# Kernel optimization log

Measured on AMD Instinct MI355X. Metric: run time of the kernel, lower is better.

## Reference

```python
import jax, jax.numpy as jnp
import numpy as np

N_NODES = 50000
N_EDGES = 800000
IN_DIM = 128
OUT_DIM = 64
NEG_SLOPE = 0.01  # torch F.leaky_relu default


def setup_inputs() -> dict:
    key = jax.random.key(0)
    k1, k2, k3, k4, k5 = jax.random.split(key, 5)
    features = jax.random.normal(k1, (N_NODES, IN_DIM), dtype=jnp.float32)
    # xavier-ish scale for weights
    fc_w = jax.random.normal(k2, (OUT_DIM, IN_DIM), dtype=jnp.float32) * (1.0 / np.sqrt(IN_DIM))
    attn_w = jax.random.normal(k3, (2 * OUT_DIM,), dtype=jnp.float32) * (1.0 / np.sqrt(2 * OUT_DIM))
    src = jax.random.randint(k4, (N_EDGES,), 0, N_NODES, dtype=jnp.int32)
    dst = jax.random.randint(k5, (N_EDGES,), 0, N_NODES, dtype=jnp.int32)
    return {"features": features, "fc_w": fc_w, "attn_w": attn_w, "src": src, "dst": dst}


def reference(features, fc_w, attn_w, src, dst):
    n = features.shape[0]
    out_dim = fc_w.shape[0]
    # z = fc(features), [N, out_dim]
    z = features @ fc_w.T
    # attn_fc([z_src || z_dst]) = z_src @ w_src + z_dst @ w_dst
    a_src = z @ attn_w[:out_dim]   # [N]
    a_dst = z @ attn_w[out_dim:]   # [N]
    e = a_src[src] + a_dst[dst]    # [E] per-edge raw score
    e = jnp.where(e > 0, e, NEG_SLOPE * e)  # leaky_relu
    # edge softmax over incoming edges of each dst node
    e_max = jax.ops.segment_max(e, dst, num_segments=n)      # [N]
    w = jnp.exp(e - e_max[dst])                               # [E]
    denom = jax.ops.segment_sum(w, dst, num_segments=n)       # [N]
    # weighted neighbor sum: sum_e alpha_e * z[src_e]
    num = jax.ops.segment_sum(w[:, None] * z[src], dst, num_segments=n)  # [N, out_dim]
    h = num / jnp.where(denom > 0, denom, 1.0)[:, None]
    # activation = elu
    h = jax.nn.elu(h)
    return h
```

## Files before the change

kernel.cpp:

```cpp
#include <hip/hip_runtime.h>
#include <hip/hip_bf16.h>
#include <hip/hip_fp16.h>

#define N_NODES 50000
#define N_EDGES 800000
#define IN_DIM 128
#define OUT_DIM 64
#define NEG_SLOPE 0.01f
#define NEG_INF (-3.0e38f)

#define N_STRIPS (N_NODES / 16)
#define Z_BLOCKS ((N_STRIPS + 3) / 4)
#define E_I4 (N_EDGES / 4)

#define NB ((N_NODES + 127) / 128)
#define CAP_B 3072
#define CNT_STRIDE 16
#define EB 100
#define CHUNK_I4 (E_I4 / EB)

typedef __bf16 bf16x8 __attribute__((ext_vector_type(8)));
typedef float f32x4 __attribute__((ext_vector_type(4)));

__device__ __forceinline__ unsigned short f2bf_us(float f) {
  __hip_bfloat16 h = __float2bfloat16(f);
  return *reinterpret_cast<unsigned short*>(&h);
}
__device__ __forceinline__ bf16x8 pack_bf16(float4 lo, float4 hi) {
  union { bf16x8 v; unsigned short u[8]; } r;
  r.u[0] = f2bf_us(lo.x); r.u[1] = f2bf_us(lo.y);
  r.u[2] = f2bf_us(lo.z); r.u[3] = f2bf_us(lo.w);
  r.u[4] = f2bf_us(hi.x); r.u[5] = f2bf_us(hi.y);
  r.u[6] = f2bf_us(hi.z); r.u[7] = f2bf_us(hi.w);
  return r.v;
}
__device__ __forceinline__ float bflo(unsigned u) {
  return __uint_as_float(u << 16);
}
__device__ __forceinline__ float bfhi(unsigned u) {
  return __uint_as_float(u & 0xffff0000u);
}

__global__ __launch_bounds__(256) void gat_z_bucket(
    const float* __restrict__ feat, const float* __restrict__ fcw,
    const float* __restrict__ attnw, __hip_bfloat16* __restrict__ z,
    float* __restrict__ asrc, float* __restrict__ adst,
    const int* __restrict__ src, const int* __restrict__ dst,
    int* __restrict__ cnt, unsigned* __restrict__ pairs) {
  if (blockIdx.x >= Z_BLOCKS) {
    __shared__ int hist[NB];
    __shared__ int curs[NB];
    const int tid = threadIdx.x;
    const int i0 = (blockIdx.x - Z_BLOCKS) * CHUNK_I4;
    for (int i = tid; i < NB; i += 256) hist[i] = 0;
    __syncthreads();
    for (int t = i0 + tid; t < i0 + CHUNK_I4; t += 256) {
      int4 d = ((const int4*)dst)[t];
      atomicAdd(&hist[d.x >> 7], 1);
      atomicAdd(&hist[d.y >> 7], 1);
      atomicAdd(&hist[d.z >> 7], 1);
      atomicAdd(&hist[d.w >> 7], 1);
    }
    __syncthreads();
    for (int i = tid; i < NB; i += 256) {
      int h = hist[i];
      curs[i] = h ? atomicAdd(cnt + i * CNT_STRIDE, h) : 0;
    }
    __syncthreads();
    for (int t = i0 + tid; t < i0 + CHUNK_I4; t += 256) {
      int4 s = ((const int4*)src)[t];
      int4 d = ((const int4*)dst)[t];
#define BKT_PUT(dd, ss)                                                    \
  {                                                                        \
    int b = (dd) >> 7;                                                     \
    int r = atomicAdd(&curs[b], 1);                                        \
    if (r < CAP_B)                                                         \
      pairs[(size_t)b * CAP_B + r] =                                       \
          ((unsigned)((dd) & 127) << 16) | (unsigned)(ss);                 \
  }
      BKT_PUT(d.x, s.x)
      BKT_PUT(d.y, s.y)
      BKT_PUT(d.z, s.z)
      BKT_PUT(d.w, s.w)
#undef BKT_PUT
    }
    return;
  }

  const int lane = threadIdx.x & 63;
  const int m = lane & 15;
  const int quad = lane >> 4;
  const int wv = blockIdx.x * 4 + (threadIdx.x >> 6);
  if (wv >= N_STRIPS) return;
  const int n0 = wv * 16;

  bf16x8 bfrag[4][4];
#pragma unroll
  for (int t = 0; t < 4; ++t) {
    const float* wr = fcw + (size_t)(m + 16 * t) * IN_DIM + quad * 8;
#pragma unroll
    for (int c = 0; c < 4; ++c) {
      float4 lo = *(const float4*)(wr + c * 32);
      float4 hi = *(const float4*)(wr + c * 32 + 4);
      bfrag[t][c] = pack_bf16(lo, hi);
    }
  }

  f32x4 acc[4] = {{0.f, 0.f, 0.f, 0.f}, {0.f, 0.f, 0.f, 0.f},
                  {0.f, 0.f, 0.f, 0.f}, {0.f, 0.f, 0.f, 0.f}};
  const float* ar = feat + (size_t)(n0 + m) * IN_DIM + quad * 8;
#pragma unroll
  for (int c = 0; c < 4; ++c) {
    float4 lo = *(const float4*)(ar + c * 32);
    float4 hi = *(const float4*)(ar + c * 32 + 4);
    const bf16x8 af = pack_bf16(lo, hi);
#pragma unroll
    for (int t = 0; t < 4; ++t)
      acc[t] = __builtin_amdgcn_mfma_f32_16x16x32_bf16(af, bfrag[t][c],
                                                       acc[t], 0, 0, 0);
  }

#pragma unroll
  for (int t = 0; t < 4; ++t)
#pragma unroll
    for (int r = 0; r < 4; ++r)
      z[(size_t)(n0 + quad * 4 + r) * OUT_DIM + m + 16 * t] =
          __float2bfloat16(acc[t][r]);

  float aws[4], awd[4];
#pragma unroll
  for (int t = 0; t < 4; ++t) {
    aws[t] = attnw[m + 16 * t];
    awd[t] = attnw[OUT_DIM + m + 16 * t];
  }
  float ps[4], pd[4];
#pragma unroll
  for (int r = 0; r < 4; ++r) {
    float s = 0.f, d = 0.f;
#pragma unroll
    for (int t = 0; t < 4; ++t) {
      s = fmaf(acc[t][r], aws[t], s);
      d = fmaf(acc[t][r], awd[t], d);
    }
    ps[r] = s;
    pd[r] = d;
  }
#pragma unroll
  for (int off = 1; off < 16; off <<= 1) {
#pragma unroll
    for (int r = 0; r < 4; ++r) {
      ps[r] += __shfl_xor(ps[r], off, 64);
      pd[r] += __shfl_xor(pd[r], off, 64);
    }
  }
  if (m == 0) {
#pragma unroll
    for (int r = 0; r < 4; ++r) {
      asrc[n0 + quad * 4 + r] = ps[r];
      adst[n0 + quad * 4 + r] = pd[r];
    }
  }
}

__global__ __launch_bounds__(256) void gat_build_csr(
    const unsigned* __restrict__ pairs, const int* __restrict__ cnt,
    int* __restrict__ offsets, int* __restrict__ ssorted) {
  __shared__ int hist[128], exo[128], cur[128], wsum[4];
  const int b = blockIdx.x;
  const int tid = threadIdx.x;

  int ls = 0;
  for (int i = tid; i < b; i += 256) ls += cnt[i * CNT_STRIDE];
#pragma unroll
  for (int off = 32; off; off >>= 1) ls += __shfl_xor(ls, off, 64);
  if ((tid & 63) == 0) wsum[tid >> 6] = ls;
  if (tid < 128) hist[tid] = 0;
  __syncthreads();
  const int base = wsum[0] + wsum[1] + wsum[2] + wsum[3];

  const int c = min(cnt[b * CNT_STRIDE], CAP_B);
  const unsigned* bp = pairs + (size_t)b * CAP_B;
  for (int i = tid; i < c; i += 256) atomicAdd(&hist[bp[i] >> 16], 1);
  __syncthreads();

  if (tid < 128) exo[tid] = hist[tid];
  __syncthreads();
  for (int off = 1; off < 128; off <<= 1) {
    int u = (tid >= off && tid < 128) ? exo[tid - off] : 0;
    __syncthreads();
    if (tid < 128) exo[tid] += u;
    __syncthreads();
  }
  if (tid < 128) {
    const int ex = exo[tid] - hist[tid];
    cur[tid] = ex;
    const int node = b * 128 + tid;
    if (node < N_NODES) offsets[node] = base + ex;
  }
  if (b == NB - 1 && tid == 0) offsets[N_NODES] = base + c;
  __syncthreads();

  for (int i = tid; i < c; i += 256) {
    const unsigned p = bp[i];
    const int r = atomicAdd(&cur[p >> 16], 1);
    ssorted[base + r] = (int)(p & 0xFFFFu);
  }
}

__global__ __launch_bounds__(256) void gat_agg(
    const __hip_bfloat16* __restrict__ zb, const float* __restrict__ asrc,
    const float* __restrict__ adst, const int* __restrict__ offsets,
    const int* __restrict__ ssorted, float* __restrict__ out) {
  const int lane = threadIdx.x & 63;
  const int j = lane & 7;
  const int eg = lane >> 3;
  const int node = (blockIdx.x * blockDim.x + threadIdx.x) >> 6;
  if (node >= N_NODES) return;
  const uint4* __restrict__ zp4 = (const uint4*)zb;
  const int o0 = offsets[node];
  const int o1 = offsets[node + 1];
  float4* __restrict__ orow = (float4*)(out + (size_t)node * OUT_DIM);
  if (o0 == o1) {
    if (eg == 0) {
      const float4 zv = {0.f, 0.f, 0.f, 0.f};
      orow[2 * j] = zv;
      orow[2 * j + 1] = zv;
    }
    return;
  }
  const float ad = adst[node];

  float m = NEG_INF, dsum = 0.f;
  float acca[8] = {0.f, 0.f, 0.f, 0.f, 0.f, 0.f, 0.f, 0.f};
  float accb[8] = {0.f, 0.f, 0.f, 0.f, 0.f, 0.f, 0.f, 0.f};

  for (int base = o0; base < o1; base += 64) {
    const int cnt = min(64, o1 - base);
    int s = 0;
    float ev = NEG_INF;
    if (lane < cnt) {
      s = ssorted[base + lane];
      float v = asrc[s] + ad;
      ev = v > 0.f ? v : NEG_SLOPE * v;
    }
    float cm = ev;
#pragma unroll
    for (int off = 32; off; off >>= 1) cm = fmaxf(cm, __shfl_xor(cm, off, 64));
    const float nm = fmaxf(m, cm);
    const float scale = __expf(m - nm);
    dsum *= scale;
#pragma unroll
    for (int c = 0; c < 8; ++c) {
      acca[c] *= scale;
      accb[c] *= scale;
    }
    m = nm;

    const float w = (lane < cnt) ? __expf(ev - m) : 0.f;
    dsum += w;
    const unsigned pk =
        (unsigned)s |
        ((unsigned)__half_as_ushort(__float2half(w)) << 16);

    const int ngr = (cnt + 7) >> 3;
    for (int g = 0; g < ngr; g += 2) {
      const unsigned pa = __shfl(pk, 8 * g + eg, 64);
      const int sa = (int)(pa & 0xFFFFu);
      const float wa = __half2float(__ushort_as_half((unsigned short)(pa >> 16)));
      const uint4 ua = zp4[(size_t)sa * 8 + j];
      if (g + 1 < ngr) {
        const unsigned pb = __shfl(pk, 8 * (g + 1) + eg, 64);
        const int sb = (int)(pb & 0xFFFFu);
        const float wb =
            __half2float(__ushort_as_half((unsigned short)(pb >> 16)));
        const uint4 ub = zp4[(size_t)sb * 8 + j];
        accb[0] = fmaf(wb, bflo(ub.x), accb[0]);
        accb[1] = fmaf(wb, bfhi(ub.x), accb[1]);
        accb[2] = fmaf(wb, bflo(ub.y), accb[2]);
        accb[3] = fmaf(wb, bfhi(ub.y), accb[3]);
        accb[4] = fmaf(wb, bflo(ub.z), accb[4]);
        accb[5] = fmaf(wb, bfhi(ub.z), accb[5]);
        accb[6] = fmaf(wb, bflo(ub.w), accb[6]);
        accb[7] = fmaf(wb, bfhi(ub.w), accb[7]);
      }
      acca[0] = fmaf(wa, bflo(ua.x), acca[0]);
      acca[1] = fmaf(wa, bfhi(ua.x), acca[1]);
      acca[2] = fmaf(wa, bflo(ua.y), acca[2]);
      acca[3] = fmaf(wa, bfhi(ua.y), acca[3]);
      acca[4] = fmaf(wa, bflo(ua.z), acca[4]);
      acca[5] = fmaf(wa, bfhi(ua.z), acca[5]);
      acca[6] = fmaf(wa, bflo(ua.w), acca[6]);
      acca[7] = fmaf(wa, bfhi(ua.w), acca[7]);
    }
  }

  float acc[8];
#pragma unroll
  for (int c = 0; c < 8; ++c) acc[c] = acca[c] + accb[c];
#pragma unroll
  for (int off = 8; off < 64; off <<= 1)
#pragma unroll
    for (int c = 0; c < 8; ++c) acc[c] += __shfl_xor(acc[c], off, 64);
#pragma unroll
  for (int off = 32; off; off >>= 1) dsum += __shfl_xor(dsum, off, 64);

  if (eg == 0) {
    const float inv = 1.f / (dsum > 0.f ? dsum : 1.f);
    float4 r0, r1;
    float h;
    h = acc[0] * inv; r0.x = h > 0.f ? h : expm1f(h);
    h = acc[1] * inv; r0.y = h > 0.f ? h : expm1f(h);
    h = acc[2] * inv; r0.z = h > 0.f ? h : expm1f(h);
    h = acc[3] * inv; r0.w = h > 0.f ? h : expm1f(h);
    h = acc[4] * inv; r1.x = h > 0.f ? h : expm1f(h);
    h = acc[5] * inv; r1.y = h > 0.f ? h : expm1f(h);
    h = acc[6] * inv; r1.z = h > 0.f ? h : expm1f(h);
    h = acc[7] * inv; r1.w = h > 0.f ? h : expm1f(h);
    orow[2 * j] = r0;
    orow[2 * j + 1] = r1;
  }
}

extern "C" void kernel_launch(void* const* d_in, const int* in_sizes, int n_in,
                              void* d_out, int out_size, void* d_ws, size_t ws_size,
                              hipStream_t stream) {
  const float* feat  = (const float*)d_in[0];
  const float* fcw   = (const float*)d_in[1];
  const float* attnw = (const float*)d_in[2];
  const int* src     = (const int*)d_in[3];
  const int* dst     = (const int*)d_in[4];
  float* out = (float*)d_out;

  char* ws = (char*)d_ws;
  __hip_bfloat16* z = (__hip_bfloat16*)ws;
  ws += (size_t)N_NODES * OUT_DIM * sizeof(__hip_bfloat16);
  float* asrc = (float*)ws;   ws += (size_t)N_NODES * sizeof(float);
  float* adst = (float*)ws;   ws += (size_t)N_NODES * sizeof(float);
  int* cnt = (int*)ws;        ws += (size_t)NB * CNT_STRIDE * sizeof(int);
  int* offsets = (int*)ws;    ws += (size_t)(N_NODES + 4) * sizeof(int);
  unsigned* pairs = (unsigned*)ws; ws += (size_t)NB * CAP_B * sizeof(unsigned);
  int* ssorted = (int*)ws;    ws += (size_t)N_EDGES * sizeof(int);

  hipMemsetAsync(cnt, 0, (size_t)NB * CNT_STRIDE * sizeof(int), stream);

  gat_z_bucket<<<Z_BLOCKS + EB, 256, 0, stream>>>(
      feat, fcw, attnw, z, asrc, adst, src, dst, cnt, pairs);
  gat_build_csr<<<NB, 256, 0, stream>>>(pairs, cnt, offsets, ssorted);
  gat_agg<<<(N_NODES * 64 + 255) / 256, 256, 0, stream>>>(z, asrc, adst,
                                                          offsets, ssorted, out);
}
```

Measured before the change: 145.8 us.

## Fuse CSR build and aggregation into one kernel with LDS-local sorted edges

Merges the CSR-building kernel and the aggregation kernel into a single kernel in which each block takes a 64-node bucket, counting-sorts its edges into LDS, gathers asrc values into LDS, and runs a three-pass (max, exp-sum, weighted sum) softmax aggregation per node. This removes one launch and the global round trip of offsets and the sorted source array, and drops the online-rescaling and fp16 weight packing. In exchange, buckets shrink to 64 nodes with a capacity of 1600 edges, and each block's waves handle 16 nodes serially, which lowers parallelism and loses the two-way gather unroll.

Result: slower. 166.1 us (+13.9%).

```diff
diff --git a/kernel.cpp b/kernel.cpp
--- a/kernel.cpp
+++ b/kernel.cpp
@@ -1,6 +1,5 @@
 #include <hip/hip_runtime.h>
 #include <hip/hip_bf16.h>
-#include <hip/hip_fp16.h>
 
 #define N_NODES 50000
 #define N_EDGES 800000
@@ -13,8 +12,9 @@
 #define Z_BLOCKS ((N_STRIPS + 3) / 4)
 #define E_I4 (N_EDGES / 4)
 
-#define NB ((N_NODES + 127) / 128)
-#define CAP_B 3072
+#define B_NODES 64
+#define NB ((N_NODES + B_NODES - 1) / B_NODES)
+#define CAP_B 1600
 #define CNT_STRIDE 16
 #define EB 100
 #define CHUNK_I4 (E_I4 / EB)
@@ -56,10 +56,10 @@
     __syncthreads();
     for (int t = i0 + tid; t < i0 + CHUNK_I4; t += 256) {
       int4 d = ((const int4*)dst)[t];
-      atomicAdd(&hist[d.x >> 7], 1);
-      atomicAdd(&hist[d.y >> 7], 1);
-      atomicAdd(&hist[d.z >> 7], 1);
-      atomicAdd(&hist[d.w >> 7], 1);
+      atomicAdd(&hist[d.x >> 6], 1);
+      atomicAdd(&hist[d.y >> 6], 1);
+      atomicAdd(&hist[d.z >> 6], 1);
+      atomicAdd(&hist[d.w >> 6], 1);
     }
     __syncthreads();
     for (int i = tid; i < NB; i += 256) {
@@ -72,11 +72,11 @@
       int4 d = ((const int4*)dst)[t];
 #define BKT_PUT(dd, ss)                                                    \
   {                                                                        \
-    int b = (dd) >> 7;                                                     \
+    int b = (dd) >> 6;                                                     \
     int r = atomicAdd(&curs[b], 1);                                        \
     if (r < CAP_B)                                                         \
       pairs[(size_t)b * CAP_B + r] =                                       \
-          ((unsigned)((dd) & 127) << 16) | (unsigned)(ss);                 \
+          ((unsigned)((dd) & 63) << 16) | (unsigned)(ss);                  \
   }
       BKT_PUT(d.x, s.x)
       BKT_PUT(d.y, s.y)
@@ -162,162 +162,142 @@
   }
 }
 
-__global__ __launch_bounds__(256) void gat_build_csr(
+__global__ __launch_bounds__(256) void gat_build_agg(
     const unsigned* __restrict__ pairs, const int* __restrict__ cnt,
-    int* __restrict__ offsets, int* __restrict__ ssorted) {
-  __shared__ int hist[128], exo[128], cur[128], wsum[4];
+    const float* __restrict__ asrc, const float* __restrict__ adst,
+    const __hip_bfloat16* __restrict__ zb, float* __restrict__ out) {
+  __shared__ int hist[B_NODES], exo[B_NODES], cur[B_NODES];
+  __shared__ unsigned short lsorted[CAP_B];
+  __shared__ float avs[CAP_B];
+  __shared__ float adl[B_NODES];
   const int b = blockIdx.x;
   const int tid = threadIdx.x;
-
-  int ls = 0;
-  for (int i = tid; i < b; i += 256) ls += cnt[i * CNT_STRIDE];
-#pragma unroll
-  for (int off = 32; off; off >>= 1) ls += __shfl_xor(ls, off, 64);
-  if ((tid & 63) == 0) wsum[tid >> 6] = ls;
-  if (tid < 128) hist[tid] = 0;
-  __syncthreads();
-  const int base = wsum[0] + wsum[1] + wsum[2] + wsum[3];
+  const int lane = tid & 63;
+  const int wv = tid >> 6;
+
+  if (tid < B_NODES) {
+    hist[tid] = 0;
+    const int node = b * B_NODES + tid;
+    adl[tid] = (node < N_NODES) ? adst[node] : 0.f;
+  }
+  __syncthreads();
 
   const int c = min(cnt[b * CNT_STRIDE], CAP_B);
   const unsigned* bp = pairs + (size_t)b * CAP_B;
   for (int i = tid; i < c; i += 256) atomicAdd(&hist[bp[i] >> 16], 1);
   __syncthreads();
 
-  if (tid < 128) exo[tid] = hist[tid];
-  __syncthreads();
-  for (int off = 1; off < 128; off <<= 1) {
-    int u = (tid >= off && tid < 128) ? exo[tid - off] : 0;
-    __syncthreads();
-    if (tid < 128) exo[tid] += u;
-    __syncthreads();
-  }
-  if (tid < 128) {
-    const int ex = exo[tid] - hist[tid];
-    cur[tid] = ex;
-    const int node = b * 128 + tid;
-    if (node < N_NODES) offsets[node] = base + ex;
-  }
-  if (b == NB - 1 && tid == 0) offsets[N_NODES] = base + c;
+  if (wv == 0) {
+    const int v = hist[lane];
+    int incl = v;
+#pragma unroll
+    for (int off = 1; off < 64; off <<= 1) {
+      int u = __shfl_up(incl, off, 64);
+      if (lane >= off) incl += u;
+    }
+    exo[lane] = incl - v;
+    cur[lane] = incl - v;
+  }
   __syncthreads();
 
   for (int i = tid; i < c; i += 256) {
     const unsigned p = bp[i];
     const int r = atomicAdd(&cur[p >> 16], 1);
-    ssorted[base + r] = (int)(p & 0xFFFFu);
-  }
-}
-
-__global__ __launch_bounds__(256) void gat_agg(
-    const __hip_bfloat16* __restrict__ zb, const float* __restrict__ asrc,
-    const float* __restrict__ adst, const int* __restrict__ offsets,
-    const int* __restrict__ ssorted, float* __restrict__ out) {
-  const int lane = threadIdx.x & 63;
+    lsorted[r] = (unsigned short)(p & 0xFFFFu);
+  }
+  __syncthreads();
+
+  for (int i = tid; i < c; i += 256) avs[i] = asrc[lsorted[i]];
+  __syncthreads();
+
+  const uint4* __restrict__ zp4 = (const uint4*)zb;
   const int j = lane & 7;
   const int eg = lane >> 3;
-  const int node = (blockIdx.x * blockDim.x + threadIdx.x) >> 6;
-  if (node >= N_NODES) return;
-  const uint4* __restrict__ zp4 = (const uint4*)zb;
-  const int o0 = offsets[node];
-  const int o1 = offsets[node + 1];
-  float4* __restrict__ orow = (float4*)(out + (size_t)node * OUT_DIM);
-  if (o0 == o1) {
+
+#pragma unroll 1
+  for (int it = 0; it < 16; ++it) {
+    const int ln = 4 * it + wv;
+    const int node = b * B_NODES + ln;
+    if (node >= N_NODES) continue;
+    const int base = exo[ln];
+    const int cn = hist[ln];
+    float4* __restrict__ orow = (float4*)(out + (size_t)node * OUT_DIM);
+    if (cn == 0) {
+      if (eg == 0) {
+        const float4 zv = {0.f, 0.f, 0.f, 0.f};
+        orow[2 * j] = zv;
+        orow[2 * j + 1] = zv;
+      }
+      continue;
+    }
+    const float ad = adl[ln];
+
+    float m = NEG_INF;
+    for (int e0 = 0; e0 < cn; e0 += 64) {
+      const int e = e0 + lane;
+      float ev = NEG_INF;
+      if (e < cn) {
+        const float v = avs[base + e] + ad;
+        ev = v > 0.f ? v : NEG_SLOPE * v;
+        avs[base + e] = ev;
+      }
+#pragma unroll
+      for (int off = 32; off; off >>= 1)
+        ev = fmaxf(ev, __shfl_xor(ev, off, 64));
+      m = fmaxf(m, ev);
+    }
+    float dsum = 0.f;
+    for (int e0 = 0; e0 < cn; e0 += 64) {
+      const int e = e0 + lane;
+      float w = 0.f;
+      if (e < cn) {
+        w = __expf(avs[base + e] - m);
+        avs[base + e] = w;
+      }
+      dsum += w;
+    }
+#pragma unroll
+    for (int off = 32; off; off >>= 1) dsum += __shfl_xor(dsum, off, 64);
+
+    float acc[8] = {0.f, 0.f, 0.f, 0.f, 0.f, 0.f, 0.f, 0.f};
+    for (int e0 = 0; e0 < cn; e0 += 8) {
+      const int e = e0 + eg;
+      float w = 0.f;
+      int s = 0;
+      if (e < cn) {
+        w = avs[base + e];
+        s = lsorted[base + e];
+      }
+      const uint4 u = zp4[(size_t)s * 8 + j];
+      acc[0] = fmaf(w, bflo(u.x), acc[0]);
+      acc[1] = fmaf(w, bfhi(u.x), acc[1]);
+      acc[2] = fmaf(w, bflo(u.y), acc[2]);
+      acc[3] = fmaf(w, bfhi(u.y), acc[3]);
+      acc[4] = fmaf(w, bflo(u.z), acc[4]);
+      acc[5] = fmaf(w, bfhi(u.z), acc[5]);
+      acc[6] = fmaf(w, bflo(u.w), acc[6]);
+      acc[7] = fmaf(w, bfhi(u.w), acc[7]);
+    }
+#pragma unroll
+    for (int off = 8; off < 64; off <<= 1)
+#pragma unroll
+      for (int c8 = 0; c8 < 8; ++c8) acc[c8] += __shfl_xor(acc[c8], off, 64);
+
     if (eg == 0) {
-      const float4 zv = {0.f, 0.f, 0.f, 0.f};
-      orow[2 * j] = zv;
-      orow[2 * j + 1] = zv;
-    }
-    return;
-  }
-  const float ad = adst[node];
-
-  float m = NEG_INF, dsum = 0.f;
-  float acca[8] = {0.f, 0.f, 0.f, 0.f, 0.f, 0.f, 0.f, 0.f};
-  float accb[8] = {0.f, 0.f, 0.f, 0.f, 0.f, 0.f, 0.f, 0.f};
-
-  for (int base = o0; base < o1; base += 64) {
-    const int cnt = min(64, o1 - base);
-    int s = 0;
-    float ev = NEG_INF;
-    if (lane < cnt) {
-      s = ssorted[base + lane];
-      float v = asrc[s] + ad;
-      ev = v > 0.f ? v : NEG_SLOPE * v;
-    }
-    float cm = ev;
-#pragma unroll
-    for (int off = 32; off; off >>= 1) cm = fmaxf(cm, __shfl_xor(cm, off, 64));
-    const float nm = fmaxf(m, cm);
-    const float scale = __expf(m - nm);
-    dsum *= scale;
-#pragma unroll
-    for (int c = 0; c < 8; ++c) {
-      acca[c] *= scale;
-      accb[c] *= scale;
-    }
-    m = nm;
-
-    const float w = (lane < cnt) ? __expf(ev - m) : 0.f;
-    dsum += w;
-    const unsigned pk =
-        (unsigned)s |
-        ((unsigned)__half_as_ushort(__float2half(w)) << 16);
-
-    const int ngr = (cnt + 7) >> 3;
-    for (int g = 0; g < ngr; g += 2) {
-      const unsigned pa = __shfl(pk, 8 * g + eg, 64);
-      const int sa = (int)(pa & 0xFFFFu);
-      const float wa = __half2float(__ushort_as_half((unsigned short)(pa >> 16)));
-      const uint4 ua = zp4[(size_t)sa * 8 + j];
-      if (g + 1 < ngr) {
-        const unsigned pb = __shfl(pk, 8 * (g + 1) + eg, 64);
-        const int sb = (int)(pb & 0xFFFFu);
-        const float wb =
-            __half2float(__ushort_as_half((unsigned short)(pb >> 16)));
-        const uint4 ub = zp4[(size_t)sb * 8 + j];
-        accb[0] = fmaf(wb, bflo(ub.x), accb[0]);
-        accb[1] = fmaf(wb, bfhi(ub.x), accb[1]);
-        accb[2] = fmaf(wb, bflo(ub.y), accb[2]);
-        accb[3] = fmaf(wb, bfhi(ub.y), accb[3]);
-        accb[4] = fmaf(wb, bflo(ub.z), accb[4]);
-        accb[5] = fmaf(wb, bfhi(ub.z), accb[5]);
-        accb[6] = fmaf(wb, bflo(ub.w), accb[6]);
-        accb[7] = fmaf(wb, bfhi(ub.w), accb[7]);
-      }
-      acca[0] = fmaf(wa, bflo(ua.x), acca[0]);
-      acca[1] = fmaf(wa, bfhi(ua.x), acca[1]);
-      acca[2] = fmaf(wa, bflo(ua.y), acca[2]);
-      acca[3] = fmaf(wa, bfhi(ua.y), acca[3]);
-      acca[4] = fmaf(wa, bflo(ua.z), acca[4]);
-      acca[5] = fmaf(wa, bfhi(ua.z), acca[5]);
-      acca[6] = fmaf(wa, bflo(ua.w), acca[6]);
-      acca[7] = fmaf(wa, bfhi(ua.w), acca[7]);
-    }
-  }
-
-  float acc[8];
-#pragma unroll
-  for (int c = 0; c < 8; ++c) acc[c] = acca[c] + accb[c];
-#pragma unroll
-  for (int off = 8; off < 64; off <<= 1)
-#pragma unroll
-    for (int c = 0; c < 8; ++c) acc[c] += __shfl_xor(acc[c], off, 64);
-#pragma unroll
-  for (int off = 32; off; off >>= 1) dsum += __shfl_xor(dsum, off, 64);
-
-  if (eg == 0) {
-    const float inv = 1.f / (dsum > 0.f ? dsum : 1.f);
-    float4 r0, r1;
-    float h;
-    h = acc[0] * inv; r0.x = h > 0.f ? h : expm1f(h);
-    h = acc[1] * inv; r0.y = h > 0.f ? h : expm1f(h);
-    h = acc[2] * inv; r0.z = h > 0.f ? h : expm1f(h);
-    h = acc[3] * inv; r0.w = h > 0.f ? h : expm1f(h);
-    h = acc[4] * inv; r1.x = h > 0.f ? h : expm1f(h);
-    h = acc[5] * inv; r1.y = h > 0.f ? h : expm1f(h);
-    h = acc[6] * inv; r1.z = h > 0.f ? h : expm1f(h);
-    h = acc[7] * inv; r1.w = h > 0.f ? h : expm1f(h);
-    orow[2 * j] = r0;
-    orow[2 * j + 1] = r1;
+      const float inv = 1.f / (dsum > 0.f ? dsum : 1.f);
+      float4 r0, r1;
+      float h;
+      h = acc[0] * inv; r0.x = h > 0.f ? h : expm1f(h);
+      h = acc[1] * inv; r0.y = h > 0.f ? h : expm1f(h);
+      h = acc[2] * inv; r0.z = h > 0.f ? h : expm1f(h);
+      h = acc[3] * inv; r0.w = h > 0.f ? h : expm1f(h);
+      h = acc[4] * inv; r1.x = h > 0.f ? h : expm1f(h);
+      h = acc[5] * inv; r1.y = h > 0.f ? h : expm1f(h);
+      h = acc[6] * inv; r1.z = h > 0.f ? h : expm1f(h);
+      h = acc[7] * inv; r1.w = h > 0.f ? h : expm1f(h);
+      orow[2 * j] = r0;
+      orow[2 * j + 1] = r1;
+    }
   }
 }
 
@@ -337,15 +317,11 @@
   float* asrc = (float*)ws;   ws += (size_t)N_NODES * sizeof(float);
   float* adst = (float*)ws;   ws += (size_t)N_NODES * sizeof(float);
   int* cnt = (int*)ws;        ws += (size_t)NB * CNT_STRIDE * sizeof(int);
-  int* offsets = (int*)ws;    ws += (size_t)(N_NODES + 4) * sizeof(int);
   unsigned* pairs = (unsigned*)ws; ws += (size_t)NB * CAP_B * sizeof(unsigned);
-  int* ssorted = (int*)ws;    ws += (size_t)N_EDGES * sizeof(int);
 
   hipMemsetAsync(cnt, 0, (size_t)NB * CNT_STRIDE * sizeof(int), stream);
 
   gat_z_bucket<<<Z_BLOCKS + EB, 256, 0, stream>>>(
       feat, fcw, attnw, z, asrc, adst, src, dst, cnt, pairs);
-  gat_build_csr<<<NB, 256, 0, stream>>>(pairs, cnt, offsets, ssorted);
-  gat_agg<<<(N_NODES * 64 + 255) / 256, 256, 0, stream>>>(z, asrc, adst,
-                                                          offsets, ssorted, out);
-}
+  gat_build_agg<<<NB, 256, 0, stream>>>(pairs, cnt, asrc, adst, z, out);
+}
```
